# Kernel tuning notes

Measured on AMD Instinct MI355X. Metric: run time of the kernel, lower is better.

## Reference

```python
import jax, jax.numpy as jnp
import numpy as np

N_NODES = 50000
N_EDGES = 800000
D_IN = 64
D_OUT = 64
N_LAYERS = 3


def setup_inputs() -> dict:
    key = jax.random.key(0)
    ks = jax.random.split(key, 8)
    x = jax.random.normal(ks[0], (N_NODES, D_IN), dtype=jnp.float32)
    edge_index = jax.random.randint(ks[1], (2, N_EDGES), 0, N_NODES, dtype=jnp.int64)
    s = 1.0 / np.sqrt(D_IN)
    lin1_w = jax.random.uniform(ks[2], (N_LAYERS, D_OUT, D_IN), jnp.float32, -s, s)
    lin2_w = jax.random.uniform(ks[3], (N_LAYERS, D_OUT, D_IN), jnp.float32, -s, s)
    root_w = jax.random.uniform(ks[4], (N_LAYERS, D_OUT, D_IN), jnp.float32, -s, s)
    root_b = jax.random.uniform(ks[5], (N_LAYERS, D_OUT), jnp.float32, -s, s)
    d_cat = D_IN + N_LAYERS * D_OUT
    sf = 1.0 / np.sqrt(d_cat)
    final_w = jax.random.uniform(ks[6], (D_OUT, d_cat), jnp.float32, -sf, sf)
    final_b = jax.random.uniform(ks[7], (D_OUT,), jnp.float32, -sf, sf)
    return {"x": x, "edge_index": edge_index, "lin1_w": lin1_w, "lin2_w": lin2_w,
            "root_w": root_w, "root_b": root_b, "final_w": final_w, "final_b": final_b}


def _seg_mean(vals, idx, n):
    # scatter-mean: sum then divide by degree (clamped to 1, PyG convention)
    s = jax.ops.segment_sum(vals, idx, num_segments=n)
    c = jax.ops.segment_sum(jnp.ones((vals.shape[0], 1), vals.dtype), idx, num_segments=n)
    return s / jnp.clip(c, 1.0)


def reference(x, edge_index, lin1_w, lin2_w, root_w, root_b, final_w, final_b):
    src, dst = edge_index[0], edge_index[1]
    n = x.shape[0]
    xs = [x]
    h = x
    for l in range(N_LAYERS):
        # RelConv: project then gather/scatter-mean in both edge directions + root residual
        m1 = (h @ lin1_w[l].T)[src]          # [E, D_OUT] source->target messages
        out1 = _seg_mean(m1, dst, n)
        m2 = (h @ lin2_w[l].T)[dst]          # [E, D_OUT] target->source messages
        out2 = _seg_mean(m2, src, n)
        h = jax.nn.relu(h @ root_w[l].T + root_b[l] + out1 + out2)
        xs.append(h)
    cat = jnp.concatenate(xs, axis=-1)       # [N, D_IN + L*D_OUT]
    return cat @ final_w.T + final_b
```

## Files before the change

kernel.cpp:

```cpp
#include <hip/hip_runtime.h>
#include <stdint.h>

#define NDIM 64
#define SCAN_ELEMS 2048
#define NCHK 32
#define NGRP 8
#define RMAX 6272

typedef unsigned int uint;
typedef unsigned short ushort;
typedef __attribute__((ext_vector_type(8))) short bf16x8;
typedef __attribute__((ext_vector_type(4))) float f32x4;

__device__ __forceinline__ uint f2bf2(float a, float b) {
  uint ua = __float_as_uint(a);
  uint ub = __float_as_uint(b);
  ua += 0x7fffu + ((ua >> 16) & 1u);
  ub += 0x7fffu + ((ub >> 16) & 1u);
  return (ua >> 16) | (ub & 0xffff0000u);
}
__device__ __forceinline__ ushort f2bf1(float a) {
  uint u = __float_as_uint(a);
  u += 0x7fffu + ((u >> 16) & 1u);
  return (ushort)(u >> 16);
}

__global__ __launch_bounds__(256) void convx_kernel(
    const float* __restrict__ x, uint* __restrict__ xb, int n4) {
  int e = blockIdx.x * 256 + threadIdx.x;
  if (e >= n4) return;
  float4 v = ((const float4*)x)[e];
  uint2 o;
  o.x = f2bf2(v.x, v.y);
  o.y = f2bf2(v.z, v.w);
  ((uint2*)xb)[e] = o;
}

__global__ __launch_bounds__(256) void prepack_kernel(
    const float* __restrict__ rootw, const float* __restrict__ lin1,
    const float* __restrict__ lin2, const float* __restrict__ fw,
    ushort* __restrict__ cpk, ushort* __restrict__ fpk) {
  int e = blockIdx.x * 256 + threadIdx.x;
  if (e < 36864) {
    int l = e / 12288;
    int e2 = e % 12288;
    int j = e2 & 7, lane = (e2 >> 3) & 63, t = (e2 >> 9) & 3;
    int kh = (e2 >> 11) & 1, s = e2 >> 12;
    int k = kh * 32 + (lane >> 4) * 8 + j;
    int o = t * 16 + (lane & 15);
    const float* mat = (s == 0) ? rootw : (s == 1) ? lin1 : lin2;
    cpk[e] = f2bf1(mat[l * 4096 + o * 64 + k]);
  } else if (e < 36864 + 16384) {
    int e3 = e - 36864;
    int j = e3 & 7, lane = (e3 >> 3) & 63, t = (e3 >> 9) & 3;
    int kstep = e3 >> 11;
    int k = kstep * 32 + (lane >> 4) * 8 + j;
    int o = t * 16 + (lane & 15);
    fpk[e3] = f2bf1(fw[o * 256 + k]);
  }
}

__global__ __launch_bounds__(256) void hist_kernel(
    const int* __restrict__ src, const int* __restrict__ dst,
    int* __restrict__ Hd, int* __restrict__ Hs, int E, int N, int chunk) {
  int c = blockIdx.x, g = blockIdx.y, z = blockIdx.z;
  const int* key = z ? src : dst;
  int* H = z ? Hs : Hd;
  int lo = (int)((long long)N * g / NGRP);
  int hi = (int)((long long)N * (g + 1) / NGRP);
  int range = hi - lo;
  __shared__ int cnt[RMAX];
  for (int i = threadIdx.x; i < range; i += 256) cnt[i] = 0;
  __syncthreads();
  int e0 = c * chunk, e1 = min(E, e0 + chunk);
  for (int e = e0 + (int)threadIdx.x * 4; e < e1; e += 1024) {
    if (e + 4 <= e1) {
      int4 k4 = *(const int4*)(key + e);
      if (k4.x >= lo && k4.x < hi) atomicAdd(&cnt[k4.x - lo], 1);
      if (k4.y >= lo && k4.y < hi) atomicAdd(&cnt[k4.y - lo], 1);
      if (k4.z >= lo && k4.z < hi) atomicAdd(&cnt[k4.z - lo], 1);
      if (k4.w >= lo && k4.w < hi) atomicAdd(&cnt[k4.w - lo], 1);
    } else {
      for (int k = e; k < e1; ++k) {
        int v = key[k];
        if (v >= lo && v < hi) atomicAdd(&cnt[v - lo], 1);
      }
    }
  }
  __syncthreads();
  for (int i = threadIdx.x; i < range; i += 256)
    H[(size_t)c * N + lo + i] = cnt[i];
}

__global__ __launch_bounds__(256) void degsum_kernel(
    const int* __restrict__ Hd, const int* __restrict__ Hs,
    int* __restrict__ deg_d, int* __restrict__ deg_s, int N) {
  int n = blockIdx.x * 256 + threadIdx.x;
  if (n >= N) return;
  int sd = 0, ss = 0;
#pragma unroll
  for (int c = 0; c < NCHK; ++c) {
    sd += Hd[(size_t)c * N + n];
    ss += Hs[(size_t)c * N + n];
  }
  deg_d[n] = sd;
  deg_s[n] = ss;
}

__global__ __launch_bounds__(256) void scan_partial(
    const int* __restrict__ deg_d, const int* __restrict__ deg_s,
    int* __restrict__ bsum, int n, int nb) {
  const int* deg = (blockIdx.y == 0) ? deg_d : deg_s;
  int tid = threadIdx.x;
  int base = blockIdx.x * SCAN_ELEMS;
  int s = 0;
#pragma unroll
  for (int j = 0; j < 8; ++j) {
    int i = base + j * 256 + tid;
    if (i < n) s += deg[i];
  }
#pragma unroll
  for (int off = 1; off < 64; off <<= 1) s += __shfl_xor(s, off);
  __shared__ int ws[4];
  if ((tid & 63) == 0) ws[tid >> 6] = s;
  __syncthreads();
  if (tid == 0) bsum[blockIdx.y * nb + blockIdx.x] = ws[0] + ws[1] + ws[2] + ws[3];
}

__global__ __launch_bounds__(256) void scan_bsum(int* __restrict__ bsum, int nb) {
  __shared__ int sh[256];
  int tid = threadIdx.x;
  for (int h = 0; h < 2; ++h) {
    int v = (tid < nb) ? bsum[h * nb + tid] : 0;
    sh[tid] = v;
    __syncthreads();
    for (int off = 1; off < 256; off <<= 1) {
      int t = (tid >= off) ? sh[tid - off] : 0;
      __syncthreads();
      sh[tid] += t;
      __syncthreads();
    }
    if (tid < nb) bsum[h * nb + tid] = sh[tid] - v;
    __syncthreads();
  }
}

__global__ __launch_bounds__(256) void scan_final(
    const int* __restrict__ deg_d, const int* __restrict__ deg_s,
    const int* __restrict__ bsum,
    int* __restrict__ row_d, int* __restrict__ row_s, int n, int nb) {
  const int* deg = (blockIdx.y == 0) ? deg_d : deg_s;
  int* row = (blockIdx.y == 0) ? row_d : row_s;
  int tid = threadIdx.x;
  int lane = tid & 63;
  int e0 = blockIdx.x * SCAN_ELEMS + tid * 8;
  int v[8];
  int s = 0;
#pragma unroll
  for (int j = 0; j < 8; ++j) {
    int i = e0 + j;
    v[j] = (i < n) ? deg[i] : 0;
    s += v[j];
  }
  int incl = s;
#pragma unroll
  for (int off = 1; off < 64; off <<= 1) {
    int t = __shfl_up(incl, off);
    if (lane >= off) incl += t;
  }
  __shared__ int wsum[4];
  if (lane == 63) wsum[tid >> 6] = incl;
  __syncthreads();
  int woff = 0;
  int w = tid >> 6;
  for (int k = 0; k < 4; ++k)
    if (k < w) woff += wsum[k];
  int run = incl - s + woff + bsum[blockIdx.y * nb + blockIdx.x];
#pragma unroll
  for (int j = 0; j < 8; ++j) {
    int i = e0 + j;
    if (i <= n) row[i] = run;
    run += v[j];
  }
}

__global__ __launch_bounds__(256) void cursor_kernel(
    int* __restrict__ Hd, int* __restrict__ Hs,
    const int* __restrict__ row_d, const int* __restrict__ row_s, int N) {
  int n = blockIdx.x * 256 + threadIdx.x;
  if (n >= N) return;
  int rd = row_d[n], rs = row_s[n];
#pragma unroll
  for (int c = 0; c < NCHK; ++c) {
    int t = Hd[(size_t)c * N + n]; Hd[(size_t)c * N + n] = rd; rd += t;
    t = Hs[(size_t)c * N + n];     Hs[(size_t)c * N + n] = rs; rs += t;
  }
}

__global__ __launch_bounds__(256) void scatter_kernel(
    const int* __restrict__ src, const int* __restrict__ dst,
    const int* __restrict__ Hd, const int* __restrict__ Hs,
    int* __restrict__ col_d, int* __restrict__ col_s, int E, int N, int chunk) {
  int g = blockIdx.x, c = blockIdx.y, z = blockIdx.z;
  const int* key = z ? src : dst;
  const int* val = z ? dst : src;
  const int* H = z ? Hs : Hd;
  int* colp = z ? col_s : col_d;
  int lo = (int)((long long)N * g / NGRP);
  int hi = (int)((long long)N * (g + 1) / NGRP);
  int range = hi - lo;
  __shared__ int cur[RMAX];
  for (int i = threadIdx.x; i < range; i += 256)
    cur[i] = H[(size_t)c * N + lo + i];
  __syncthreads();
  int e0 = c * chunk, e1 = min(E, e0 + chunk);
  for (int e = e0 + (int)threadIdx.x * 4; e < e1; e += 1024) {
    if (e + 4 <= e1) {
      int4 k4 = *(const int4*)(key + e);
      int4 v4 = *(const int4*)(val + e);
      if (k4.x >= lo && k4.x < hi) { int p = atomicAdd(&cur[k4.x - lo], 1); colp[p] = v4.x; }
      if (k4.y >= lo && k4.y < hi) { int p = atomicAdd(&cur[k4.y - lo], 1); colp[p] = v4.y; }
      if (k4.z >= lo && k4.z < hi) { int p = atomicAdd(&cur[k4.z - lo], 1); colp[p] = v4.z; }
      if (k4.w >= lo && k4.w < hi) { int p = atomicAdd(&cur[k4.w - lo], 1); colp[p] = v4.w; }
    } else {
      for (int k = e; k < e1; ++k) {
        int kk = key[k], vv = val[k];
        if (kk >= lo && kk < hi) { int p = atomicAdd(&cur[kk - lo], 1); colp[p] = vv; }
      }
    }
  }
}


#define FMA_ACC(A, U, W) {                                                   \
    A[0] += (W) * __uint_as_float((U).x << 16);                              \
    A[1] += (W) * __uint_as_float((U).x & 0xffff0000u);                      \
    A[2] += (W) * __uint_as_float((U).y << 16);                              \
    A[3] += (W) * __uint_as_float((U).y & 0xffff0000u);                      \
    A[4] += (W) * __uint_as_float((U).z << 16);                              \
    A[5] += (W) * __uint_as_float((U).z & 0xffff0000u);                      \
    A[6] += (W) * __uint_as_float((U).w << 16);                              \
    A[7] += (W) * __uint_as_float((U).w & 0xffff0000u); }

__global__ __launch_bounds__(256) void aggv_kernel(
    const ushort* __restrict__ hB,
    const int* __restrict__ row_d, const int* __restrict__ col_d, ushort* __restrict__ g1,
    const int* __restrict__ row_s, const int* __restrict__ col_s, ushort* __restrict__ g2,
    int N, int E) {
  const int* row = (blockIdx.y == 0) ? row_d : row_s;
  const int* col = (blockIdx.y == 0) ? col_d : col_s;
  ushort* outp = (blockIdx.y == 0) ? g1 : g2;
  int wv = blockIdx.x * 4 + (threadIdx.x >> 6);
  int lane = threadIdx.x & 63;
  int g = lane >> 3;
  int fl = lane & 7;
  int node = wv * 8 + g;
  int nc = min(node, N - 1);
  int s0 = row[nc], s1 = row[nc + 1];
  int d = s1 - s0;
  int dmax = d;
  dmax = max(dmax, __shfl_xor(dmax, 8));
  dmax = max(dmax, __shfl_xor(dmax, 16));
  dmax = max(dmax, __shfl_xor(dmax, 32));
  const ushort* tab = hB + fl * 8;
  float acc[8] = {0.f, 0.f, 0.f, 0.f, 0.f, 0.f, 0.f, 0.f};
  float bcc[8] = {0.f, 0.f, 0.f, 0.f, 0.f, 0.f, 0.f, 0.f};
  int i = 0;
  for (; i + 2 <= dmax; i += 2) {
    int p0 = s0 + i, p1 = s0 + i + 1;
    float w0 = p0 < s1 ? 1.f : 0.f;
    float w1 = p1 < s1 ? 1.f : 0.f;
    int n0 = col[min(p0, E - 1)];
    int n1 = col[min(p1, E - 1)];
    uint4 u0 = *(const uint4*)(tab + (size_t)n0 * 64);
    uint4 u1 = *(const uint4*)(tab + (size_t)n1 * 64);
    FMA_ACC(acc, u0, w0);
    FMA_ACC(bcc, u1, w1);
  }
  if (i < dmax) {
    int p = s0 + i;
    float w = p < s1 ? 1.f : 0.f;
    int n = col[min(p, E - 1)];
    uint4 u = *(const uint4*)(tab + (size_t)n * 64);
    FMA_ACC(acc, u, w);
  }
#pragma unroll
  for (int k = 0; k < 8; ++k) acc[k] += bcc[k];
  float inv = d > 0 ? 1.f / (float)d : 0.f;
  if (node < N) {
    uint4 o;
    o.x = f2bf2(acc[0] * inv, acc[1] * inv);
    o.y = f2bf2(acc[2] * inv, acc[3] * inv);
    o.z = f2bf2(acc[4] * inv, acc[5] * inv);
    o.w = f2bf2(acc[6] * inv, acc[7] * inv);
    *(uint4*)(outp + (size_t)node * NDIM + fl * 8) = o;
  }
}


__global__ __launch_bounds__(256) void combine_mfma(
    const ushort* __restrict__ hB, const ushort* __restrict__ g1b,
    const ushort* __restrict__ g2b, const ushort* __restrict__ cpkL,
    const float* __restrict__ bias, ushort* __restrict__ outB, int N) {
  int tid = threadIdx.x;
  int w = tid >> 6, lane = tid & 63;
  int col = lane & 15, kg = lane >> 4;
  int nb = blockIdx.x * 64 + w * 16;
  int arow = min(nb + col, N - 1);
  f32x4 acc[4] = {{0.f,0.f,0.f,0.f},{0.f,0.f,0.f,0.f},{0.f,0.f,0.f,0.f},{0.f,0.f,0.f,0.f}};
  const ushort* srcs[3] = {hB, g1b, g2b};
#pragma unroll
  for (int s = 0; s < 3; ++s) {
    const ushort* act = srcs[s] + (size_t)arow * 64 + kg * 8;
#pragma unroll
    for (int kh = 0; kh < 2; ++kh) {
      bf16x8 av = *(const bf16x8*)(act + kh * 32);
      const bf16x8* wb = (const bf16x8*)(cpkL + (s * 2 + kh) * 2048);
#pragma unroll
      for (int t = 0; t < 4; ++t)
        acc[t] = __builtin_amdgcn_mfma_f32_16x16x32_bf16(av, wb[t * 64 + lane], acc[t], 0, 0, 0);
    }
  }
#pragma unroll
  for (int t = 0; t < 4; ++t) {
    float bv = bias[t * 16 + col];
#pragma unroll
    for (int r = 0; r < 4; ++r) {
      int node = nb + kg * 4 + r;
      if (node < N)
        outB[(size_t)node * NDIM + t * 16 + col] = f2bf1(fmaxf(acc[t][r] + bv, 0.f));
    }
  }
}


__global__ __launch_bounds__(256) void final_mfma(
    const ushort* __restrict__ xB, const ushort* __restrict__ h1B,
    const ushort* __restrict__ h2B, const ushort* __restrict__ h3B,
    const ushort* __restrict__ fpk, const float* __restrict__ fb,
    float* __restrict__ outp, int N) {
  int tid = threadIdx.x;
  int w = tid >> 6, lane = tid & 63;
  int col = lane & 15, kg = lane >> 4;
  int nb = blockIdx.x * 64 + w * 16;
  int arow = min(nb + col, N - 1);
  f32x4 acc[4] = {{0.f,0.f,0.f,0.f},{0.f,0.f,0.f,0.f},{0.f,0.f,0.f,0.f},{0.f,0.f,0.f,0.f}};
  const ushort* bufs[4] = {xB, h1B, h2B, h3B};
#pragma unroll
  for (int b = 0; b < 4; ++b) {
    const ushort* act = bufs[b] + (size_t)arow * 64 + kg * 8;
#pragma unroll
    for (int kh = 0; kh < 2; ++kh) {
      bf16x8 av = *(const bf16x8*)(act + kh * 32);
      const bf16x8* wb = (const bf16x8*)(fpk + (b * 2 + kh) * 2048);
#pragma unroll
      for (int t = 0; t < 4; ++t)
        acc[t] = __builtin_amdgcn_mfma_f32_16x16x32_bf16(av, wb[t * 64 + lane], acc[t], 0, 0, 0);
    }
  }
#pragma unroll
  for (int t = 0; t < 4; ++t) {
    float bv = fb[t * 16 + col];
#pragma unroll
    for (int r = 0; r < 4; ++r) {
      int node = nb + kg * 4 + r;
      if (node < N)
        outp[(size_t)node * NDIM + t * 16 + col] = acc[t][r] + bv;
    }
  }
}


extern "C" void kernel_launch(void* const* d_in, const int* in_sizes, int n_in,
                              void* d_out, int out_size, void* d_ws, size_t ws_size,
                              hipStream_t stream) {
  const float* x     = (const float*)d_in[0];
  const int*   ei    = (const int*)d_in[1];
  const float* lin1  = (const float*)d_in[2];
  const float* lin2  = (const float*)d_in[3];
  const float* rootw = (const float*)d_in[4];
  const float* rootb = (const float*)d_in[5];
  const float* fw    = (const float*)d_in[6];
  const float* fb    = (const float*)d_in[7];
  float* out = (float*)d_out;

  int N = in_sizes[0] / NDIM;
  int E = in_sizes[1] / 2;
  const int* src = ei;
  const int* dst = ei + E;

  int* ip = (int*)d_ws;
  int* Hd    = ip; ip += (size_t)NCHK * N;
  int* Hs    = ip; ip += (size_t)NCHK * N;
  int* deg_d = ip; ip += N;
  int* deg_s = ip; ip += N;
  int* row_d = ip; ip += N + 1;
  int* row_s = ip; ip += N + 1;
  int* bsum  = ip; ip += 256;
  int* col_d = ip; ip += E;
  int* col_s = ip; ip += E;
  uintptr_t fbase = (((uintptr_t)ip) + 255) & ~(uintptr_t)255;
  ushort* cpk = (ushort*)fbase;
  ushort* fpk = cpk + 36864;
  ushort* hB0 = fpk + 16384;
  ushort* hB1 = hB0 + (size_t)N * NDIM;
  ushort* hB2 = hB1 + (size_t)N * NDIM;
  ushort* hB3 = hB2 + (size_t)N * NDIM;
  ushort* g1b = hB3 + (size_t)N * NDIM;
  ushort* g2b = g1b + (size_t)N * NDIM;

  int chunk = (E + NCHK - 1) / NCHK;
  int nb = (N + SCAN_ELEMS - 1) / SCAN_ELEMS;
  int nblk = (N + 255) / 256;

  convx_kernel<<<(N * 16 + 255) / 256, 256, 0, stream>>>(x, (uint*)hB0, N * 16);
  prepack_kernel<<<(36864 + 16384 + 255) / 256, 256, 0, stream>>>(
      rootw, lin1, lin2, fw, cpk, fpk);
  hist_kernel<<<dim3(NCHK, NGRP, 2), 256, 0, stream>>>(src, dst, Hd, Hs, E, N, chunk);
  degsum_kernel<<<nblk, 256, 0, stream>>>(Hd, Hs, deg_d, deg_s, N);
  scan_partial<<<dim3(nb, 2), 256, 0, stream>>>(deg_d, deg_s, bsum, N, nb);
  scan_bsum<<<1, 256, 0, stream>>>(bsum, nb);
  scan_final<<<dim3(nb, 2), 256, 0, stream>>>(deg_d, deg_s, bsum, row_d, row_s, N, nb);
  cursor_kernel<<<nblk, 256, 0, stream>>>(Hd, Hs, row_d, row_s, N);
  scatter_kernel<<<dim3(NGRP, NCHK, 2), 256, 0, stream>>>(src, dst, Hd, Hs,
                                                          col_d, col_s, E, N, chunk);

  int avgrid = (N + 31) / 32;
  int g64 = (N + 63) / 64;
  ushort* hBufs[4] = {hB0, hB1, hB2, hB3};
  for (int l = 0; l < 3; ++l) {
    aggv_kernel<<<dim3(avgrid, 2), 256, 0, stream>>>(hBufs[l], row_d, col_d, g1b,
                                                     row_s, col_s, g2b, N, E);
    combine_mfma<<<g64, 256, 0, stream>>>(hBufs[l], g1b, g2b,
                                          cpk + (size_t)l * 12288,
                                          rootb + (size_t)l * 64,
                                          hBufs[l + 1], N);
  }
  final_mfma<<<g64, 256, 0, stream>>>(hB0, hB1, hB2, hB3, fpk, fb, out, N);
}
```

Baseline: 207.6 us.

## Store CSR column indices as 16-bit and use fewer, wider histogram groups

Column index arrays for both edge directions are now stored as ushort instead of int. This halves the CSR index traffic in the scatter kernel and in every aggregation pass. Separately, the histogram kernel now splits nodes into 4 groups with a larger shared-memory count array instead of 8, which halves the number of edge-reading passes it makes. The risk is that node ids up to 50000 fit in 16 bits only because N is below 65536, so the scheme does not hold for larger graphs. The bigger shared array (about 50KB) may also reduce how many histogram blocks run per CU.

```diff
diff --git a/kernel.cpp b/kernel.cpp
--- a/kernel.cpp
+++ b/kernel.cpp
@@ -5,7 +5,9 @@
 #define SCAN_ELEMS 2048
 #define NCHK 32
 #define NGRP 8
+#define NGRP_H 4
 #define RMAX 6272
+#define RMAX_H 12544
 
 typedef unsigned int uint;
 typedef unsigned short ushort;
@@ -66,10 +68,10 @@
   int c = blockIdx.x, g = blockIdx.y, z = blockIdx.z;
   const int* key = z ? src : dst;
   int* H = z ? Hs : Hd;
-  int lo = (int)((long long)N * g / NGRP);
-  int hi = (int)((long long)N * (g + 1) / NGRP);
+  int lo = (int)((long long)N * g / NGRP_H);
+  int hi = (int)((long long)N * (g + 1) / NGRP_H);
   int range = hi - lo;
-  __shared__ int cnt[RMAX];
+  __shared__ int cnt[RMAX_H];
   for (int i = threadIdx.x; i < range; i += 256) cnt[i] = 0;
   __syncthreads();
   int e0 = c * chunk, e1 = min(E, e0 + chunk);
@@ -200,12 +202,12 @@
 __global__ __launch_bounds__(256) void scatter_kernel(
     const int* __restrict__ src, const int* __restrict__ dst,
     const int* __restrict__ Hd, const int* __restrict__ Hs,
-    int* __restrict__ col_d, int* __restrict__ col_s, int E, int N, int chunk) {
+    ushort* __restrict__ col_d, ushort* __restrict__ col_s, int E, int N, int chunk) {
   int g = blockIdx.x, c = blockIdx.y, z = blockIdx.z;
   const int* key = z ? src : dst;
   const int* val = z ? dst : src;
   const int* H = z ? Hs : Hd;
-  int* colp = z ? col_s : col_d;
+  ushort* colp = z ? col_s : col_d;
   int lo = (int)((long long)N * g / NGRP);
   int hi = (int)((long long)N * (g + 1) / NGRP);
   int range = hi - lo;
@@ -218,14 +220,14 @@
     if (e + 4 <= e1) {
       int4 k4 = *(const int4*)(key + e);
       int4 v4 = *(const int4*)(val + e);
-      if (k4.x >= lo && k4.x < hi) { int p = atomicAdd(&cur[k4.x - lo], 1); colp[p] = v4.x; }
-      if (k4.y >= lo && k4.y < hi) { int p = atomicAdd(&cur[k4.y - lo], 1); colp[p] = v4.y; }
-      if (k4.z >= lo && k4.z < hi) { int p = atomicAdd(&cur[k4.z - lo], 1); colp[p] = v4.z; }
-      if (k4.w >= lo && k4.w < hi) { int p = atomicAdd(&cur[k4.w - lo], 1); colp[p] = v4.w; }
+      if (k4.x >= lo && k4.x < hi) { int p = atomicAdd(&cur[k4.x - lo], 1); colp[p] = (ushort)v4.x; }
+      if (k4.y >= lo && k4.y < hi) { int p = atomicAdd(&cur[k4.y - lo], 1); colp[p] = (ushort)v4.y; }
+      if (k4.z >= lo && k4.z < hi) { int p = atomicAdd(&cur[k4.z - lo], 1); colp[p] = (ushort)v4.z; }
+      if (k4.w >= lo && k4.w < hi) { int p = atomicAdd(&cur[k4.w - lo], 1); colp[p] = (ushort)v4.w; }
     } else {
       for (int k = e; k < e1; ++k) {
         int kk = key[k], vv = val[k];
-        if (kk >= lo && kk < hi) { int p = atomicAdd(&cur[kk - lo], 1); colp[p] = vv; }
+        if (kk >= lo && kk < hi) { int p = atomicAdd(&cur[kk - lo], 1); colp[p] = (ushort)vv; }
       }
     }
   }
@@ -244,11 +246,11 @@
 
 __global__ __launch_bounds__(256) void aggv_kernel(
     const ushort* __restrict__ hB,
-    const int* __restrict__ row_d, const int* __restrict__ col_d, ushort* __restrict__ g1,
-    const int* __restrict__ row_s, const int* __restrict__ col_s, ushort* __restrict__ g2,
+    const int* __restrict__ row_d, const ushort* __restrict__ col_d, ushort* __restrict__ g1,
+    const int* __restrict__ row_s, const ushort* __restrict__ col_s, ushort* __restrict__ g2,
     int N, int E) {
   const int* row = (blockIdx.y == 0) ? row_d : row_s;
-  const int* col = (blockIdx.y == 0) ? col_d : col_s;
+  const ushort* col = (blockIdx.y == 0) ? col_d : col_s;
   ushort* outp = (blockIdx.y == 0) ? g1 : g2;
   int wv = blockIdx.x * 4 + (threadIdx.x >> 6);
   int lane = threadIdx.x & 63;
@@ -297,7 +299,6 @@
   }
 }
 
-
 __global__ __launch_bounds__(256) void combine_mfma(
     const ushort* __restrict__ hB, const ushort* __restrict__ g1b,
     const ushort* __restrict__ g2b, const ushort* __restrict__ cpkL,
@@ -332,7 +333,6 @@
     }
   }
 }
-
 
 __global__ __launch_bounds__(256) void final_mfma(
     const ushort* __restrict__ xB, const ushort* __restrict__ h1B,
@@ -397,8 +397,8 @@
   int* row_d = ip; ip += N + 1;
   int* row_s = ip; ip += N + 1;
   int* bsum  = ip; ip += 256;
-  int* col_d = ip; ip += E;
-  int* col_s = ip; ip += E;
+  ushort* col_d = (ushort*)ip; ip += (E + 1) / 2;
+  ushort* col_s = (ushort*)ip; ip += (E + 1) / 2;
   uintptr_t fbase = (((uintptr_t)ip) + 255) & ~(uintptr_t)255;
   ushort* cpk = (ushort*)fbase;
   ushort* fpk = cpk + 36864;
@@ -416,7 +416,7 @@
   convx_kernel<<<(N * 16 + 255) / 256, 256, 0, stream>>>(x, (uint*)hB0, N * 16);
   prepack_kernel<<<(36864 + 16384 + 255) / 256, 256, 0, stream>>>(
       rootw, lin1, lin2, fw, cpk, fpk);
-  hist_kernel<<<dim3(NCHK, NGRP, 2), 256, 0, stream>>>(src, dst, Hd, Hs, E, N, chunk);
+  hist_kernel<<<dim3(NCHK, NGRP_H, 2), 256, 0, stream>>>(src, dst, Hd, Hs, E, N, chunk);
   degsum_kernel<<<nblk, 256, 0, stream>>>(Hd, Hs, deg_d, deg_s, N);
   scan_partial<<<dim3(nb, 2), 256, 0, stream>>>(deg_d, deg_s, bsum, N, nb);
   scan_bsum<<<1, 256, 0, stream>>>(bsum, nb);
```

Result: no change. 205.0 us (-1.2%).
